# Performance work log

Measured on AMD Instinct MI355X. Metric: run time of the kernel, lower is better.

Reference implementation:

```python
import jax, jax.numpy as jnp
import numpy as np

N_NODES = 50000
N_EDGES = 800000
IN_DIM = 89
HID = 128
N_CLASSES = 64
N_GRAPHS = 64


def setup_inputs() -> dict:
    key = jax.random.key(0)
    ks = jax.random.split(key, 12)
    nf = jax.random.normal(ks[0], (N_NODES, IN_DIM), dtype=jnp.float32)
    src = jax.random.randint(ks[1], (N_EDGES,), 0, N_NODES, dtype=jnp.int32)
    dst = jnp.sort(jax.random.randint(ks[2], (N_EDGES,), 0, N_NODES, dtype=jnp.int32))
    graph_id = jnp.sort(jax.random.randint(ks[3], (N_NODES,), 0, N_GRAPHS, dtype=jnp.int32))
    s = 0.05
    W1 = jax.random.normal(ks[4], (IN_DIM, HID), dtype=jnp.float32) * s
    b1 = jnp.zeros((HID,), jnp.float32)
    W2 = jax.random.normal(ks[5], (HID, HID), dtype=jnp.float32) * s
    b2 = jnp.zeros((HID,), jnp.float32)
    W3 = jax.random.normal(ks[6], (HID, HID), dtype=jnp.float32) * s
    b3 = jnp.zeros((HID,), jnp.float32)
    Wc1 = jax.random.normal(ks[7], (HID, HID), dtype=jnp.float32) * s
    bc1 = jnp.zeros((HID,), jnp.float32)
    Wc2 = jax.random.normal(ks[8], (HID, N_CLASSES), dtype=jnp.float32) * s
    bc2 = jnp.zeros((N_CLASSES,), jnp.float32)
    return {"nf": nf, "src": src, "dst": dst, "graph_id": graph_id,
            "n_graphs": N_GRAPHS,
            "W1": W1, "b1": b1, "W2": W2, "b2": b2, "W3": W3, "b3": b3,
            "Wc1": Wc1, "bc1": bc1, "Wc2": Wc2, "bc2": bc2}


def reference(nf, src, dst, graph_id, n_graphs, W1, b1, W2, b2, W3, b3, Wc1, bc1, Wc2, bc2):
    n = nf.shape[0]
    # in-degree per destination node (DGL mean over mailbox); clamp to avoid /0
    deg = jax.ops.segment_sum(jnp.ones((src.shape[0],), nf.dtype), dst, num_segments=n)
    inv_deg = (1.0 / jnp.maximum(deg, 1.0))[:, None]

    def gcn(h, W, b):
        # copy_u: gather source features per edge, mean-reduce by dst, linear+ReLU
        agg = jax.ops.segment_sum(h[src], dst, num_segments=n) * inv_deg
        return jax.nn.relu(agg @ W + b)

    h = gcn(nf, W1, b1)
    h = gcn(h, W2, b2)
    h = gcn(h, W3, b3)

    # dgl.mean_nodes: per-graph mean pool over nodes
    cnt = jax.ops.segment_sum(jnp.ones((n,), h.dtype), graph_id, num_segments=n_graphs)
    hg = jax.ops.segment_sum(h, graph_id, num_segments=n_graphs) / jnp.maximum(cnt, 1.0)[:, None]

    return jax.nn.relu(hg @ Wc1 + bc1) @ Wc2 + bc2
```

## Files before the change

### kernel.cpp

```cpp
#include <hip/hip_runtime.h>

#define N_NODES   50000
#define N_EDGES   800000
#define IN_DIM    89
#define KP1       96
#define HID       128
#define N_CLASSES 64
#define N_GRAPHS  64
#define PSPLIT    16

typedef __attribute__((ext_vector_type(8))) short bf16x8;
typedef __attribute__((ext_vector_type(4))) float f32x4;

__device__ __forceinline__ unsigned short f2bf(float x) {
    union { float f; unsigned u; } v; v.f = x;
    unsigned r = v.u + 0x7FFF + ((v.u >> 16) & 1);
    return (unsigned short)(r >> 16);
}
__device__ __forceinline__ float bf2f(unsigned short x) {
    union { unsigned u; float f; } v; v.u = ((unsigned)x) << 16;
    return v.f;
}

#define NB_ROW  196
#define NB_WT   176

__global__ void prep_kernel(const int* __restrict__ dst,
                            const int* __restrict__ gid,
                            const float* __restrict__ W1,
                            const float* __restrict__ W2,
                            const float* __restrict__ W3,
                            int* __restrict__ node_ptr,
                            int* __restrict__ graph_ptr,
                            unsigned short* __restrict__ wt1,
                            unsigned short* __restrict__ wt2,
                            unsigned short* __restrict__ wt3) {
    const int b = blockIdx.x;
    if (b < NB_ROW) {
        const int i = b * 256 + threadIdx.x;
        if (i <= N_NODES) {
            int lo = 0, hi = N_EDGES;
            while (lo < hi) { int mid = (lo + hi) >> 1; if (dst[mid] < i) lo = mid + 1; else hi = mid; }
            node_ptr[i] = lo;
        }
        if (i <= N_GRAPHS) {
            int lo = 0, hi = N_NODES;
            while (lo < hi) { int mid = (lo + hi) >> 1; if (gid[mid] < i) lo = mid + 1; else hi = mid; }
            graph_ptr[i] = lo;
        }
    } else {
        int idx = (b - NB_ROW) * 256 + threadIdx.x;
        if (idx < HID * KP1) {
            const int col = idx / KP1, k = idx - col * KP1;
            wt1[idx] = (k < IN_DIM) ? f2bf(W1[(size_t)k * HID + col]) : (unsigned short)0;
        } else if ((idx -= HID * KP1) < HID * HID) {
            const int col = idx / HID, k = idx - col * HID;
            wt2[idx] = f2bf(W2[(size_t)k * HID + col]);
        } else if ((idx -= HID * HID) < HID * HID) {
            const int col = idx / HID, k = idx - col * HID;
            wt3[idx] = f2bf(W3[(size_t)k * HID + col]);
        }
    }
}

__global__ __launch_bounds__(256) void gemm1_kernel(
        const float* __restrict__ nf,
        const unsigned short* __restrict__ WT,
        unsigned short* __restrict__ Y, int M) {
    const int wave = threadIdx.x >> 6;
    const int lane = threadIdx.x & 63;
    const int r    = lane & 15;
    const int kg   = lane >> 4;

    const int row  = blockIdx.x * 64 + wave * 16 + r;
    const int rowc = (row < M) ? row : (M - 1);

    bf16x8 afrag[3];
#pragma unroll
    for (int t = 0; t < 3; ++t) {
        const int kb = 32 * t + kg * 8;
#pragma unroll
        for (int j = 0; j < 8; ++j) {
            const int k = kb + j;
            const float v = (k < IN_DIM) ? nf[(size_t)rowc * IN_DIM + k] : 0.f;
            afrag[t][j] = (short)f2bf(v);
        }
    }

    f32x4 acc[8];
#pragma unroll
    for (int i = 0; i < 8; ++i) acc[i] = (f32x4){0.f, 0.f, 0.f, 0.f};

#pragma unroll
    for (int t = 0; t < 3; ++t) {
        const int k0 = 32 * t;
#pragma unroll
        for (int c = 0; c < 8; ++c) {
            const bf16x8 b = *reinterpret_cast<const bf16x8*>(
                WT + (size_t)(c * 16 + r) * KP1 + kg * 8 + k0);
            acc[c] = __builtin_amdgcn_mfma_f32_16x16x32_bf16(afrag[t], b, acc[c], 0, 0, 0);
        }
    }

    const int orow0 = blockIdx.x * 64 + wave * 16 + kg * 4;
#pragma unroll
    for (int c = 0; c < 8; ++c)
#pragma unroll
        for (int p = 0; p < 4; ++p) {
            const int orow = orow0 + p;
            if (orow < M) Y[(size_t)orow * HID + c * 16 + r] = f2bf(acc[c][p]);
        }
}

#define HS_STRIDE 140
__global__ __launch_bounds__(512) void fused_agg_gemm_kernel(
        const unsigned short* __restrict__ Pin,
        const int* __restrict__ src,
        const int* __restrict__ node_ptr,
        const float* __restrict__ bias,
        const unsigned short* __restrict__ WT,
        unsigned short* __restrict__ Pout) {
    __shared__ unsigned short hs[16 * HS_STRIDE];

    const int wave = threadIdx.x >> 6;
    const int lane = threadIdx.x & 63;
    const int q    = lane >> 4;
    const int g    = lane & 15;
    const int vbase = blockIdx.x * 16;

    const float4 b0 = *reinterpret_cast<const float4*>(bias + g * 8);
    const float4 b1 = *reinterpret_cast<const float4*>(bias + g * 8 + 4);

#pragma unroll
    for (int i = 0; i < 2; ++i) {
        const int li = wave * 2 + i;
        const int v  = vbase + li;
        const int lo = node_ptr[v];
        const int hi = node_ptr[v + 1];
        const float inv = 1.0f / (float)max(hi - lo, 1);

        float acc[8];
#pragma unroll
        for (int j = 0; j < 8; ++j) acc[j] = 0.f;

        int e = lo + q;
        for (; e + 12 < hi; e += 16) {
            const int u0 = src[e];
            const int u1 = src[e + 4];
            const int u2 = src[e + 8];
            const int u3 = src[e + 12];
            const bf16x8 r0 = *reinterpret_cast<const bf16x8*>(Pin + (size_t)u0 * HID + g * 8);
            const bf16x8 r1 = *reinterpret_cast<const bf16x8*>(Pin + (size_t)u1 * HID + g * 8);
            const bf16x8 r2 = *reinterpret_cast<const bf16x8*>(Pin + (size_t)u2 * HID + g * 8);
            const bf16x8 r3 = *reinterpret_cast<const bf16x8*>(Pin + (size_t)u3 * HID + g * 8);
#pragma unroll
            for (int j = 0; j < 8; ++j)
                acc[j] += (bf2f((unsigned short)r0[j]) + bf2f((unsigned short)r1[j]))
                        + (bf2f((unsigned short)r2[j]) + bf2f((unsigned short)r3[j]));
        }
        for (; e < hi; e += 4) {
            const int u = src[e];
            const bf16x8 r = *reinterpret_cast<const bf16x8*>(Pin + (size_t)u * HID + g * 8);
#pragma unroll
            for (int j = 0; j < 8; ++j) acc[j] += bf2f((unsigned short)r[j]);
        }
#pragma unroll
        for (int j = 0; j < 8; ++j) {
            acc[j] += __shfl_xor(acc[j], 16);
            acc[j] += __shfl_xor(acc[j], 32);
        }
        if (q == 0) {
            bf16x8 ob;
            ob[0] = (short)f2bf(fmaxf(acc[0] * inv + b0.x, 0.f));
            ob[1] = (short)f2bf(fmaxf(acc[1] * inv + b0.y, 0.f));
            ob[2] = (short)f2bf(fmaxf(acc[2] * inv + b0.z, 0.f));
            ob[3] = (short)f2bf(fmaxf(acc[3] * inv + b0.w, 0.f));
            ob[4] = (short)f2bf(fmaxf(acc[4] * inv + b1.x, 0.f));
            ob[5] = (short)f2bf(fmaxf(acc[5] * inv + b1.y, 0.f));
            ob[6] = (short)f2bf(fmaxf(acc[6] * inv + b1.z, 0.f));
            ob[7] = (short)f2bf(fmaxf(acc[7] * inv + b1.w, 0.f));
            *reinterpret_cast<bf16x8*>(&hs[li * HS_STRIDE + g * 8]) = ob;
        }
    }
    __syncthreads();

    const int r  = lane & 15;
    const int kg = lane >> 4;

    f32x4 acc2 = (f32x4){0.f, 0.f, 0.f, 0.f};
#pragma unroll
    for (int k0 = 0; k0 < HID; k0 += 32) {
        const bf16x8 a = *reinterpret_cast<const bf16x8*>(&hs[r * HS_STRIDE + kg * 8 + k0]);
        const bf16x8 b = *reinterpret_cast<const bf16x8*>(
            WT + (size_t)(wave * 16 + r) * HID + kg * 8 + k0);
        acc2 = __builtin_amdgcn_mfma_f32_16x16x32_bf16(a, b, acc2, 0, 0, 0);
    }

    const int orow0 = vbase + kg * 4;
#pragma unroll
    for (int p = 0; p < 4; ++p)
        Pout[(size_t)(orow0 + p) * HID + wave * 16 + r] = f2bf(acc2[p]);
}

__global__ void agg128_f32_kernel(const unsigned short* __restrict__ Pb,
                                  const int* __restrict__ src,
                                  const int* __restrict__ node_ptr,
                                  const float* __restrict__ bias,
                                  float* __restrict__ out) {
    const int wave = threadIdx.x >> 6;
    const int lane = threadIdx.x & 63;
    const int v    = blockIdx.x * 4 + wave;
    if (v >= N_NODES) return;

    const int lo = node_ptr[v];
    const int hi = node_ptr[v + 1];
    const float inv = 1.0f / (float)max(hi - lo, 1);

    const int q = lane >> 4;
    const int g = lane & 15;

    float acc[8];
#pragma unroll
    for (int j = 0; j < 8; ++j) acc[j] = 0.f;

    int e = lo + q;
    for (; e + 12 < hi; e += 16) {
        const int u0 = src[e];
        const int u1 = src[e + 4];
        const int u2 = src[e + 8];
        const int u3 = src[e + 12];
        const bf16x8 r0 = *reinterpret_cast<const bf16x8*>(Pb + (size_t)u0 * HID + g * 8);
        const bf16x8 r1 = *reinterpret_cast<const bf16x8*>(Pb + (size_t)u1 * HID + g * 8);
        const bf16x8 r2 = *reinterpret_cast<const bf16x8*>(Pb + (size_t)u2 * HID + g * 8);
        const bf16x8 r3 = *reinterpret_cast<const bf16x8*>(Pb + (size_t)u3 * HID + g * 8);
#pragma unroll
        for (int j = 0; j < 8; ++j)
            acc[j] += (bf2f((unsigned short)r0[j]) + bf2f((unsigned short)r1[j]))
                    + (bf2f((unsigned short)r2[j]) + bf2f((unsigned short)r3[j]));
    }
    for (; e < hi; e += 4) {
        const int u = src[e];
        const bf16x8 r = *reinterpret_cast<const bf16x8*>(Pb + (size_t)u * HID + g * 8);
#pragma unroll
        for (int j = 0; j < 8; ++j) acc[j] += bf2f((unsigned short)r[j]);
    }
#pragma unroll
    for (int j = 0; j < 8; ++j) {
        acc[j] += __shfl_xor(acc[j], 16);
        acc[j] += __shfl_xor(acc[j], 32);
    }

    if (q == 0) {
        const float4 b0 = *reinterpret_cast<const float4*>(bias + g * 8);
        const float4 b1 = *reinterpret_cast<const float4*>(bias + g * 8 + 4);
        float4 a = make_float4(fmaxf(acc[0] * inv + b0.x, 0.f), fmaxf(acc[1] * inv + b0.y, 0.f),
                               fmaxf(acc[2] * inv + b0.z, 0.f), fmaxf(acc[3] * inv + b0.w, 0.f));
        float4 b = make_float4(fmaxf(acc[4] * inv + b1.x, 0.f), fmaxf(acc[5] * inv + b1.y, 0.f),
                               fmaxf(acc[6] * inv + b1.z, 0.f), fmaxf(acc[7] * inv + b1.w, 0.f));
        *reinterpret_cast<float4*>(out + (size_t)v * HID + g * 8)     = a;
        *reinterpret_cast<float4*>(out + (size_t)v * HID + g * 8 + 4) = b;
    }
}

__global__ void pool_partial_kernel(const float* __restrict__ h3,
                                    const int* __restrict__ graph_ptr,
                                    float* __restrict__ hgp) {
    const int g   = blockIdx.x / PSPLIT;
    const int s   = blockIdx.x % PSPLIT;
    const int j   = threadIdx.x;
    const int lo  = graph_ptr[g];
    const int hi  = graph_ptr[g + 1];

    float acc = 0.f;
    for (int r = lo + s; r < hi; r += PSPLIT)
        acc += h3[(size_t)r * HID + j];
    hgp[(size_t)blockIdx.x * HID + j] = acc;
}

__global__ void cls_kernel(const float* __restrict__ hgp,
                           const int* __restrict__ graph_ptr,
                           const float* __restrict__ Wc1,
                           const float* __restrict__ bc1,
                           const float* __restrict__ Wc2,
                           const float* __restrict__ bc2,
                           float* __restrict__ out) {
    const int g = blockIdx.x;
    const int j = threadIdx.x;
    const int cnt = graph_ptr[g + 1] - graph_ptr[g];
    const float inv = 1.0f / (float)max(cnt, 1);

    float acc = 0.f;
#pragma unroll
    for (int s = 0; s < PSPLIT; ++s)
        acc += hgp[(size_t)(g * PSPLIT + s) * HID + j];

    __shared__ float row[HID];
    __shared__ float trow[HID];
    row[j] = acc * inv;
    __syncthreads();

    float a1 = bc1[j];
#pragma unroll 4
    for (int k = 0; k < HID; ++k) a1 = fmaf(row[k], Wc1[k * HID + j], a1);
    trow[j] = fmaxf(a1, 0.f);
    __syncthreads();

    if (j < N_CLASSES) {
        float a2 = bc2[j];
#pragma unroll 4
        for (int k = 0; k < HID; ++k) a2 = fmaf(trow[k], Wc2[k * N_CLASSES + j], a2);
        out[g * N_CLASSES + j] = a2;
    }
}

extern "C" void kernel_launch(void* const* d_in, const int* in_sizes, int n_in,
                              void* d_out, int out_size, void* d_ws, size_t ws_size,
                              hipStream_t stream) {
    const float* nf   = (const float*)d_in[0];
    const int*   src  = (const int*)  d_in[1];
    const int*   dst  = (const int*)  d_in[2];
    const int*   gid  = (const int*)  d_in[3];
    const float* W1  = (const float*)d_in[5];
    const float* b1  = (const float*)d_in[6];
    const float* W2  = (const float*)d_in[7];
    const float* b2  = (const float*)d_in[8];
    const float* W3  = (const float*)d_in[9];
    const float* b3  = (const float*)d_in[10];
    const float* Wc1 = (const float*)d_in[11];
    const float* bc1 = (const float*)d_in[12];
    const float* Wc2 = (const float*)d_in[13];
    const float* bc2 = (const float*)d_in[14];
    float* out = (float*)d_out;

    char* ws = (char*)d_ws;
    size_t off = 0;
    auto alloc = [&](size_t bytes) { void* p = ws + off; off = (off + bytes + 255) & ~(size_t)255; return p; };
    int*   node_ptr  = (int*)  alloc((N_NODES + 1) * sizeof(int));
    int*   graph_ptr = (int*)  alloc((N_GRAPHS + 1) * sizeof(int));
    float* h3        = (float*)alloc((size_t)N_NODES * HID * sizeof(float));
    unsigned short* PbA = (unsigned short*)alloc((size_t)N_NODES * HID * sizeof(unsigned short));
    unsigned short* PbB = (unsigned short*)alloc((size_t)N_NODES * HID * sizeof(unsigned short));
    unsigned short* wt1 = (unsigned short*)alloc((size_t)HID * KP1 * sizeof(unsigned short));
    unsigned short* wt2 = (unsigned short*)alloc((size_t)HID * HID * sizeof(unsigned short));
    unsigned short* wt3 = (unsigned short*)alloc((size_t)HID * HID * sizeof(unsigned short));
    float* hgp       = (float*)alloc((size_t)N_GRAPHS * PSPLIT * HID * sizeof(float));
    (void)ws_size;

    const int GEMM_GRID  = (N_NODES + 63) / 64;
    const int FUSED_GRID = N_NODES / 16;
    const int AGG_GRID   = (N_NODES + 3) / 4;

    prep_kernel<<<NB_ROW + NB_WT, 256, 0, stream>>>(
        dst, gid, W1, W2, W3, node_ptr, graph_ptr, wt1, wt2, wt3);

    gemm1_kernel<<<GEMM_GRID, 256, 0, stream>>>(nf, wt1, PbA, N_NODES);

    fused_agg_gemm_kernel<<<FUSED_GRID, 512, 0, stream>>>(PbA, src, node_ptr, b1, wt2, PbB);

    fused_agg_gemm_kernel<<<FUSED_GRID, 512, 0, stream>>>(PbB, src, node_ptr, b2, wt3, PbA);

    agg128_f32_kernel<<<AGG_GRID, 256, 0, stream>>>(PbA, src, node_ptr, b3, h3);

    pool_partial_kernel<<<N_GRAPHS * PSPLIT, HID, 0, stream>>>(h3, graph_ptr, hgp);
    cls_kernel<<<N_GRAPHS, HID, 0, stream>>>(hgp, graph_ptr, Wc1, bc1, Wc2, bc2, out);
}
```

Before: 179.9 us.

## Process one node per wave in fused aggregate-GEMM, dropping LDS staging and barrier

The fused aggregation+GEMM kernel now assigns one destination node per wave, with 256-thread blocks, instead of 16 nodes per 512-thread block. The aggregated row is broadcast through lane shuffles into the MFMA A operand, so the shared-memory tile and the block barrier go away. Because all 16 MFMA rows hold the same node, each wave issues 32 MFMAs per node. Each wave also re-reads the full 128x128 weight matrix per node. That greatly increases MFMA and cache traffic in exchange for finer load balancing and no synchronisation.

```diff
diff --git a/kernel.cpp b/kernel.cpp
--- a/kernel.cpp
+++ b/kernel.cpp
@@ -112,94 +112,94 @@
         }
 }
 
-#define HS_STRIDE 140
-__global__ __launch_bounds__(512) void fused_agg_gemm_kernel(
+__global__ __launch_bounds__(256) void fused_agg_gemm_kernel(
         const unsigned short* __restrict__ Pin,
         const int* __restrict__ src,
         const int* __restrict__ node_ptr,
         const float* __restrict__ bias,
         const unsigned short* __restrict__ WT,
         unsigned short* __restrict__ Pout) {
-    __shared__ unsigned short hs[16 * HS_STRIDE];
-
     const int wave = threadIdx.x >> 6;
     const int lane = threadIdx.x & 63;
     const int q    = lane >> 4;
     const int g    = lane & 15;
-    const int vbase = blockIdx.x * 16;
+    const int v    = blockIdx.x * 4 + wave;
+
+    const int lo = node_ptr[v];
+    const int hi = node_ptr[v + 1];
+    const float inv = 1.0f / (float)max(hi - lo, 1);
+
+    float acc[8];
+#pragma unroll
+    for (int j = 0; j < 8; ++j) acc[j] = 0.f;
+
+    int e = lo + q;
+    for (; e + 12 < hi; e += 16) {
+        const int u0 = src[e];
+        const int u1 = src[e + 4];
+        const int u2 = src[e + 8];
+        const int u3 = src[e + 12];
+        const bf16x8 r0 = *reinterpret_cast<const bf16x8*>(Pin + (size_t)u0 * HID + g * 8);
+        const bf16x8 r1 = *reinterpret_cast<const bf16x8*>(Pin + (size_t)u1 * HID + g * 8);
+        const bf16x8 r2 = *reinterpret_cast<const bf16x8*>(Pin + (size_t)u2 * HID + g * 8);
+        const bf16x8 r3 = *reinterpret_cast<const bf16x8*>(Pin + (size_t)u3 * HID + g * 8);
+#pragma unroll
+        for (int j = 0; j < 8; ++j)
+            acc[j] += (bf2f((unsigned short)r0[j]) + bf2f((unsigned short)r1[j]))
+                    + (bf2f((unsigned short)r2[j]) + bf2f((unsigned short)r3[j]));
+    }
+    for (; e < hi; e += 4) {
+        const int u = src[e];
+        const bf16x8 r = *reinterpret_cast<const bf16x8*>(Pin + (size_t)u * HID + g * 8);
+#pragma unroll
+        for (int j = 0; j < 8; ++j) acc[j] += bf2f((unsigned short)r[j]);
+    }
+#pragma unroll
+    for (int j = 0; j < 8; ++j) {
+        acc[j] += __shfl_xor(acc[j], 16);
+        acc[j] += __shfl_xor(acc[j], 32);
+    }
 
     const float4 b0 = *reinterpret_cast<const float4*>(bias + g * 8);
     const float4 b1 = *reinterpret_cast<const float4*>(bias + g * 8 + 4);
-
-#pragma unroll
-    for (int i = 0; i < 2; ++i) {
-        const int li = wave * 2 + i;
-        const int v  = vbase + li;
-        const int lo = node_ptr[v];
-        const int hi = node_ptr[v + 1];
-        const float inv = 1.0f / (float)max(hi - lo, 1);
-
-        float acc[8];
-#pragma unroll
-        for (int j = 0; j < 8; ++j) acc[j] = 0.f;
-
-        int e = lo + q;
-        for (; e + 12 < hi; e += 16) {
-            const int u0 = src[e];
-            const int u1 = src[e + 4];
-            const int u2 = src[e + 8];
-            const int u3 = src[e + 12];
-            const bf16x8 r0 = *reinterpret_cast<const bf16x8*>(Pin + (size_t)u0 * HID + g * 8);
-            const bf16x8 r1 = *reinterpret_cast<const bf16x8*>(Pin + (size_t)u1 * HID + g * 8);
-            const bf16x8 r2 = *reinterpret_cast<const bf16x8*>(Pin + (size_t)u2 * HID + g * 8);
-            const bf16x8 r3 = *reinterpret_cast<const bf16x8*>(Pin + (size_t)u3 * HID + g * 8);
-#pragma unroll
-            for (int j = 0; j < 8; ++j)
-                acc[j] += (bf2f((unsigned short)r0[j]) + bf2f((unsigned short)r1[j]))
-                        + (bf2f((unsigned short)r2[j]) + bf2f((unsigned short)r3[j]));
-        }
-        for (; e < hi; e += 4) {
-            const int u = src[e];
-            const bf16x8 r = *reinterpret_cast<const bf16x8*>(Pin + (size_t)u * HID + g * 8);
-#pragma unroll
-            for (int j = 0; j < 8; ++j) acc[j] += bf2f((unsigned short)r[j]);
-        }
-#pragma unroll
-        for (int j = 0; j < 8; ++j) {
-            acc[j] += __shfl_xor(acc[j], 16);
-            acc[j] += __shfl_xor(acc[j], 32);
-        }
-        if (q == 0) {
-            bf16x8 ob;
-            ob[0] = (short)f2bf(fmaxf(acc[0] * inv + b0.x, 0.f));
-            ob[1] = (short)f2bf(fmaxf(acc[1] * inv + b0.y, 0.f));
-            ob[2] = (short)f2bf(fmaxf(acc[2] * inv + b0.z, 0.f));
-            ob[3] = (short)f2bf(fmaxf(acc[3] * inv + b0.w, 0.f));
-            ob[4] = (short)f2bf(fmaxf(acc[4] * inv + b1.x, 0.f));
-            ob[5] = (short)f2bf(fmaxf(acc[5] * inv + b1.y, 0.f));
-            ob[6] = (short)f2bf(fmaxf(acc[6] * inv + b1.z, 0.f));
-            ob[7] = (short)f2bf(fmaxf(acc[7] * inv + b1.w, 0.f));
-            *reinterpret_cast<bf16x8*>(&hs[li * HS_STRIDE + g * 8]) = ob;
-        }
-    }
-    __syncthreads();
-
-    const int r  = lane & 15;
-    const int kg = lane >> 4;
-
-    f32x4 acc2 = (f32x4){0.f, 0.f, 0.f, 0.f};
-#pragma unroll
-    for (int k0 = 0; k0 < HID; k0 += 32) {
-        const bf16x8 a = *reinterpret_cast<const bf16x8*>(&hs[r * HS_STRIDE + kg * 8 + k0]);
-        const bf16x8 b = *reinterpret_cast<const bf16x8*>(
-            WT + (size_t)(wave * 16 + r) * HID + kg * 8 + k0);
-        acc2 = __builtin_amdgcn_mfma_f32_16x16x32_bf16(a, b, acc2, 0, 0, 0);
-    }
-
-    const int orow0 = vbase + kg * 4;
-#pragma unroll
-    for (int p = 0; p < 4; ++p)
-        Pout[(size_t)(orow0 + p) * HID + wave * 16 + r] = f2bf(acc2[p]);
+    bf16x8 ob;
+    ob[0] = (short)f2bf(fmaxf(acc[0] * inv + b0.x, 0.f));
+    ob[1] = (short)f2bf(fmaxf(acc[1] * inv + b0.y, 0.f));
+    ob[2] = (short)f2bf(fmaxf(acc[2] * inv + b0.z, 0.f));
+    ob[3] = (short)f2bf(fmaxf(acc[3] * inv + b0.w, 0.f));
+    ob[4] = (short)f2bf(fmaxf(acc[4] * inv + b1.x, 0.f));
+    ob[5] = (short)f2bf(fmaxf(acc[5] * inv + b1.y, 0.f));
+    ob[6] = (short)f2bf(fmaxf(acc[6] * inv + b1.z, 0.f));
+    ob[7] = (short)f2bf(fmaxf(acc[7] * inv + b1.w, 0.f));
+    const int4 obi = *reinterpret_cast<const int4*>(&ob);
+
+#pragma unroll
+    for (int p = 0; p < 2; ++p) {
+        f32x4 dacc[4];
+#pragma unroll
+        for (int c = 0; c < 4; ++c) dacc[c] = (f32x4){0.f, 0.f, 0.f, 0.f};
+
+#pragma unroll
+        for (int t = 0; t < 4; ++t) {
+            const int sg = 4 * t + q;
+            int4 ai;
+            ai.x = __shfl(obi.x, sg);
+            ai.y = __shfl(obi.y, sg);
+            ai.z = __shfl(obi.z, sg);
+            ai.w = __shfl(obi.w, sg);
+            const bf16x8 a = *reinterpret_cast<const bf16x8*>(&ai);
+#pragma unroll
+            for (int c = 0; c < 4; ++c) {
+                const int cout = (p * 4 + c) * 16 + g;
+                const bf16x8 b = *reinterpret_cast<const bf16x8*>(
+                    WT + (size_t)cout * HID + q * 8 + 32 * t);
+                dacc[c] = __builtin_amdgcn_mfma_f32_16x16x32_bf16(a, b, dacc[c], 0, 0, 0);
+            }
+        }
+        float val = (q == 0) ? dacc[0][0] : (q == 1) ? dacc[1][0]
+                  : (q == 2) ? dacc[2][0] : dacc[3][0];
+        Pout[(size_t)v * HID + (p * 4 + q) * 16 + g] = f2bf(val);
+    }
 }
 
 __global__ void agg128_f32_kernel(const unsigned short* __restrict__ Pb,
@@ -347,7 +347,7 @@
     (void)ws_size;
 
     const int GEMM_GRID  = (N_NODES + 63) / 64;
-    const int FUSED_GRID = N_NODES / 16;
+    const int FUSED_GRID = N_NODES / 4;
     const int AGG_GRID   = (N_NODES + 3) / 4;
 
     prep_kernel<<<NB_ROW + NB_WT, 256, 0, stream>>>(
@@ -355,9 +355,9 @@
 
     gemm1_kernel<<<GEMM_GRID, 256, 0, stream>>>(nf, wt1, PbA, N_NODES);
 
-    fused_agg_gemm_kernel<<<FUSED_GRID, 512, 0, stream>>>(PbA, src, node_ptr, b1, wt2, PbB);
-
-    fused_agg_gemm_kernel<<<FUSED_GRID, 512, 0, stream>>>(PbB, src, node_ptr, b2, wt3, PbA);
+    fused_agg_gemm_kernel<<<FUSED_GRID, 256, 0, stream>>>(PbA, src, node_ptr, b1, wt2, PbB);
+
+    fused_agg_gemm_kernel<<<FUSED_GRID, 256, 0, stream>>>(PbB, src, node_ptr, b2, wt3, PbA);
 
     agg128_f32_kernel<<<AGG_GRID, 256, 0, stream>>>(PbA, src, node_ptr, b3, h3);
 
```

Measured after the change: 473.7 us, median of 2. 2.63x slower.

## Fuse prep with first GEMM and use dynamic node scheduling in fused agg-GEMM

Applied to the files above, without the earlier changes.

Merges the prep kernel and the first GEMM into one launch. Each GEMM block now converts W1 to a bf16 transposed tile in shared memory itself, so the separate wt1 buffer and its launch go away. The fused aggregate+GEMM kernel drops from 512 to 256 threads. Its waves pull node indices from a shared atomic counter to balance uneven degrees, and each wave computes two MFMA column tiles. The cost is redundant W1 conversion in every GEMM block plus atomic and barrier overhead, and each block now has fewer waves to hide gather latency.

```diff
diff --git a/kernel.cpp b/kernel.cpp
--- a/kernel.cpp
+++ b/kernel.cpp
@@ -23,18 +23,25 @@
 }
 
 #define NB_ROW  196
-#define NB_WT   176
-
-__global__ void prep_kernel(const int* __restrict__ dst,
-                            const int* __restrict__ gid,
-                            const float* __restrict__ W1,
-                            const float* __restrict__ W2,
-                            const float* __restrict__ W3,
-                            int* __restrict__ node_ptr,
-                            int* __restrict__ graph_ptr,
-                            unsigned short* __restrict__ wt1,
-                            unsigned short* __restrict__ wt2,
-                            unsigned short* __restrict__ wt3) {
+#define NB_WT2  128
+#define NB_PRE  (NB_ROW + NB_WT2)
+#define GEMM1_GRID ((N_NODES + 63) / 64)
+#define WS1 100
+
+__global__ __launch_bounds__(256) void prep_gemm1_kernel(
+        const int* __restrict__ dst,
+        const int* __restrict__ gid,
+        const float* __restrict__ W1,
+        const float* __restrict__ W2,
+        const float* __restrict__ W3,
+        const float* __restrict__ nf,
+        int* __restrict__ node_ptr,
+        int* __restrict__ graph_ptr,
+        unsigned short* __restrict__ wt2,
+        unsigned short* __restrict__ wt3,
+        unsigned short* __restrict__ Y) {
+    __shared__ unsigned short wt1s[HID * WS1];
+
     const int b = blockIdx.x;
     if (b < NB_ROW) {
         const int i = b * 256 + threadIdx.x;
@@ -48,32 +55,36 @@
             while (lo < hi) { int mid = (lo + hi) >> 1; if (gid[mid] < i) lo = mid + 1; else hi = mid; }
             graph_ptr[i] = lo;
         }
-    } else {
+        return;
+    }
+    if (b < NB_PRE) {
         int idx = (b - NB_ROW) * 256 + threadIdx.x;
-        if (idx < HID * KP1) {
-            const int col = idx / KP1, k = idx - col * KP1;
-            wt1[idx] = (k < IN_DIM) ? f2bf(W1[(size_t)k * HID + col]) : (unsigned short)0;
-        } else if ((idx -= HID * KP1) < HID * HID) {
+        if (idx < HID * HID) {
             const int col = idx / HID, k = idx - col * HID;
             wt2[idx] = f2bf(W2[(size_t)k * HID + col]);
-        } else if ((idx -= HID * HID) < HID * HID) {
+        } else {
+            idx -= HID * HID;
             const int col = idx / HID, k = idx - col * HID;
             wt3[idx] = f2bf(W3[(size_t)k * HID + col]);
         }
-    }
-}
-
-__global__ __launch_bounds__(256) void gemm1_kernel(
-        const float* __restrict__ nf,
-        const unsigned short* __restrict__ WT,
-        unsigned short* __restrict__ Y, int M) {
-    const int wave = threadIdx.x >> 6;
-    const int lane = threadIdx.x & 63;
+        return;
+    }
+
+    const int tid = threadIdx.x;
+    for (int idx = tid; idx < KP1 * HID; idx += 256) {
+        const int k = idx >> 7, col = idx & 127;
+        const float v = (k < IN_DIM) ? W1[(size_t)k * HID + col] : 0.f;
+        wt1s[col * WS1 + k] = f2bf(v);
+    }
+    __syncthreads();
+
+    const int wave = tid >> 6;
+    const int lane = tid & 63;
     const int r    = lane & 15;
     const int kg   = lane >> 4;
 
-    const int row  = blockIdx.x * 64 + wave * 16 + r;
-    const int rowc = (row < M) ? row : (M - 1);
+    const int row  = (b - NB_PRE) * 64 + wave * 16 + r;
+    const int rowc = (row < N_NODES) ? row : (N_NODES - 1);
 
     bf16x8 afrag[3];
 #pragma unroll
@@ -93,47 +104,52 @@
 
 #pragma unroll
     for (int t = 0; t < 3; ++t) {
-        const int k0 = 32 * t;
 #pragma unroll
         for (int c = 0; c < 8; ++c) {
-            const bf16x8 b = *reinterpret_cast<const bf16x8*>(
-                WT + (size_t)(c * 16 + r) * KP1 + kg * 8 + k0);
-            acc[c] = __builtin_amdgcn_mfma_f32_16x16x32_bf16(afrag[t], b, acc[c], 0, 0, 0);
-        }
-    }
-
-    const int orow0 = blockIdx.x * 64 + wave * 16 + kg * 4;
+            const bf16x8 bb = *reinterpret_cast<const bf16x8*>(
+                &wt1s[(c * 16 + r) * WS1 + kg * 8 + 32 * t]);
+            acc[c] = __builtin_amdgcn_mfma_f32_16x16x32_bf16(afrag[t], bb, acc[c], 0, 0, 0);
+        }
+    }
+
+    const int orow0 = (b - NB_PRE) * 64 + wave * 16 + kg * 4;
 #pragma unroll
     for (int c = 0; c < 8; ++c)
 #pragma unroll
         for (int p = 0; p < 4; ++p) {
             const int orow = orow0 + p;
-            if (orow < M) Y[(size_t)orow * HID + c * 16 + r] = f2bf(acc[c][p]);
-        }
-}
-
-#define HS_STRIDE 140
-__global__ __launch_bounds__(512) void fused_agg_gemm_kernel(
+            if (orow < N_NODES) Y[(size_t)orow * HID + c * 16 + r] = f2bf(acc[c][p]);
+        }
+}
+
+__global__ __launch_bounds__(256) void fused_agg_gemm_kernel(
         const unsigned short* __restrict__ Pin,
         const int* __restrict__ src,
         const int* __restrict__ node_ptr,
         const float* __restrict__ bias,
         const unsigned short* __restrict__ WT,
         unsigned short* __restrict__ Pout) {
-    __shared__ unsigned short hs[16 * HS_STRIDE];
-
-    const int wave = threadIdx.x >> 6;
-    const int lane = threadIdx.x & 63;
+    __shared__ unsigned short hs[16][136];
+    __shared__ int cnt;
+
+    const int tid  = threadIdx.x;
+    const int lane = tid & 63;
     const int q    = lane >> 4;
     const int g    = lane & 15;
     const int vbase = blockIdx.x * 16;
 
+    if (tid == 0) cnt = 0;
+    __syncthreads();
+
     const float4 b0 = *reinterpret_cast<const float4*>(bias + g * 8);
     const float4 b1 = *reinterpret_cast<const float4*>(bias + g * 8 + 4);
 
-#pragma unroll
-    for (int i = 0; i < 2; ++i) {
-        const int li = wave * 2 + i;
+    for (;;) {
+        int li;
+        if (lane == 0) li = atomicAdd(&cnt, 1);
+        li = __shfl(li, 0);
+        if (li >= 16) break;
+
         const int v  = vbase + li;
         const int lo = node_ptr[v];
         const int hi = node_ptr[v + 1];
@@ -179,27 +195,39 @@
             ob[5] = (short)f2bf(fmaxf(acc[5] * inv + b1.y, 0.f));
             ob[6] = (short)f2bf(fmaxf(acc[6] * inv + b1.z, 0.f));
             ob[7] = (short)f2bf(fmaxf(acc[7] * inv + b1.w, 0.f));
-            *reinterpret_cast<bf16x8*>(&hs[li * HS_STRIDE + g * 8]) = ob;
-        }
-    }
-    __syncthreads();
-
+            *reinterpret_cast<bf16x8*>(&hs[li][g * 8]) = ob;
+        }
+    }
+    __syncthreads();
+
+    const int wave = tid >> 6;
     const int r  = lane & 15;
     const int kg = lane >> 4;
 
-    f32x4 acc2 = (f32x4){0.f, 0.f, 0.f, 0.f};
+    f32x4 acc2[2];
+#pragma unroll
+    for (int t = 0; t < 2; ++t) acc2[t] = (f32x4){0.f, 0.f, 0.f, 0.f};
+
 #pragma unroll
     for (int k0 = 0; k0 < HID; k0 += 32) {
-        const bf16x8 a = *reinterpret_cast<const bf16x8*>(&hs[r * HS_STRIDE + kg * 8 + k0]);
-        const bf16x8 b = *reinterpret_cast<const bf16x8*>(
-            WT + (size_t)(wave * 16 + r) * HID + kg * 8 + k0);
-        acc2 = __builtin_amdgcn_mfma_f32_16x16x32_bf16(a, b, acc2, 0, 0, 0);
+        const bf16x8 a = *reinterpret_cast<const bf16x8*>(&hs[r][kg * 8 + k0]);
+#pragma unroll
+        for (int t = 0; t < 2; ++t) {
+            const int nf = wave * 2 + t;
+            const bf16x8 b = *reinterpret_cast<const bf16x8*>(
+                WT + (size_t)(nf * 16 + r) * HID + kg * 8 + k0);
+            acc2[t] = __builtin_amdgcn_mfma_f32_16x16x32_bf16(a, b, acc2[t], 0, 0, 0);
+        }
     }
 
     const int orow0 = vbase + kg * 4;
 #pragma unroll
-    for (int p = 0; p < 4; ++p)
-        Pout[(size_t)(orow0 + p) * HID + wave * 16 + r] = f2bf(acc2[p]);
+    for (int t = 0; t < 2; ++t) {
+        const int nf = wave * 2 + t;
+#pragma unroll
+        for (int p = 0; p < 4; ++p)
+            Pout[(size_t)(orow0 + p) * HID + nf * 16 + r] = f2bf(acc2[t][p]);
+    }
 }
 
 __global__ void agg128_f32_kernel(const unsigned short* __restrict__ Pb,
@@ -340,24 +368,20 @@
     float* h3        = (float*)alloc((size_t)N_NODES * HID * sizeof(float));
     unsigned short* PbA = (unsigned short*)alloc((size_t)N_NODES * HID * sizeof(unsigned short));
     unsigned short* PbB = (unsigned short*)alloc((size_t)N_NODES * HID * sizeof(unsigned short));
-    unsigned short* wt1 = (unsigned short*)alloc((size_t)HID * KP1 * sizeof(unsigned short));
     unsigned short* wt2 = (unsigned short*)alloc((size_t)HID * HID * sizeof(unsigned short));
     unsigned short* wt3 = (unsigned short*)alloc((size_t)HID * HID * sizeof(unsigned short));
     float* hgp       = (float*)alloc((size_t)N_GRAPHS * PSPLIT * HID * sizeof(float));
     (void)ws_size;
 
-    const int GEMM_GRID  = (N_NODES + 63) / 64;
     const int FUSED_GRID = N_NODES / 16;
     const int AGG_GRID   = (N_NODES + 3) / 4;
 
-    prep_kernel<<<NB_ROW + NB_WT, 256, 0, stream>>>(
-        dst, gid, W1, W2, W3, node_ptr, graph_ptr, wt1, wt2, wt3);
-
-    gemm1_kernel<<<GEMM_GRID, 256, 0, stream>>>(nf, wt1, PbA, N_NODES);
-
-    fused_agg_gemm_kernel<<<FUSED_GRID, 512, 0, stream>>>(PbA, src, node_ptr, b1, wt2, PbB);
-
-    fused_agg_gemm_kernel<<<FUSED_GRID, 512, 0, stream>>>(PbB, src, node_ptr, b2, wt3, PbA);
+    prep_gemm1_kernel<<<NB_PRE + GEMM1_GRID, 256, 0, stream>>>(
+        dst, gid, W1, W2, W3, nf, node_ptr, graph_ptr, wt2, wt3, PbA);
+
+    fused_agg_gemm_kernel<<<FUSED_GRID, 256, 0, stream>>>(PbA, src, node_ptr, b1, wt2, PbB);
+
+    fused_agg_gemm_kernel<<<FUSED_GRID, 256, 0, stream>>>(PbB, src, node_ptr, b2, wt3, PbA);
 
     agg128_f32_kernel<<<AGG_GRID, 256, 0, stream>>>(PbA, src, node_ptr, b3, h3);
 
```

After: 177.3 us. About the same (-1.4%).
